# Performance work log

Hardware: AMD Instinct MI355X
Metric: run time of the kernel (lower is better)

The kernel has to match this reference:

```python
import jax, jax.numpy as jnp
import numpy as np

N_NODES = 50000
N_EDGES = 800000
IN_C = 64
HID = 64
OUT_C = 64
N_GRAPHS = 64


def setup_inputs() -> dict:
    key = jax.random.key(0)
    ks = jax.random.split(key, 12)
    x = jax.random.normal(ks[0], (N_NODES, IN_C), dtype=jnp.float32)
    edge_index = jax.random.randint(ks[1], (2, N_EDGES), 0, N_NODES, dtype=jnp.int64)
    # sorted graph-id vector guaranteed to cover all N_GRAPHS segments
    batch = (jnp.arange(N_NODES, dtype=jnp.int64) * N_GRAPHS) // N_NODES
    s = 0.1
    W1_root = jax.random.normal(ks[2], (IN_C, HID), dtype=jnp.float32) * s
    W1_rel = jax.random.normal(ks[3], (IN_C, HID), dtype=jnp.float32) * s
    b1 = jnp.zeros((HID,), dtype=jnp.float32)
    W2_root = jax.random.normal(ks[4], (HID, OUT_C), dtype=jnp.float32) * s
    W2_rel = jax.random.normal(ks[5], (HID, OUT_C), dtype=jnp.float32) * s
    b2 = jnp.zeros((OUT_C,), dtype=jnp.float32)
    fc1_w = jax.random.normal(ks[6], (OUT_C, 8), dtype=jnp.float32) * s
    fc1_b = jnp.zeros((8,), dtype=jnp.float32)
    fc2_w = jax.random.normal(ks[7], (8, 2), dtype=jnp.float32) * s
    fc2_b = jnp.zeros((2,), dtype=jnp.float32)
    return {
        "x": x, "edge_index": edge_index, "batch": batch,
        "W1_root": W1_root, "W1_rel": W1_rel, "b1": b1,
        "W2_root": W2_root, "W2_rel": W2_rel, "b2": b2,
        "fc1_w": fc1_w, "fc1_b": fc1_b, "fc2_w": fc2_w, "fc2_b": fc2_b,
    }


def _graph_conv(h, src, dst, W_root, W_rel, b, n_nodes):
    # PyG GraphConv (aggr='add'): out_i = W_root h_i + W_rel * sum_{j->i} h_j + b
    agg = jax.ops.segment_sum(h[src], dst, num_segments=n_nodes)
    return h @ W_root + agg @ W_rel + b


def reference(x, edge_index, batch, W1_root, W1_rel, b1,
              W2_root, W2_rel, b2, fc1_w, fc1_b, fc2_w, fc2_b):
    n = x.shape[0]
    src, dst = edge_index[0], edge_index[1]
    h = jax.nn.relu(_graph_conv(x, src, dst, W1_root, W1_rel, b1, n))
    h = jax.nn.relu(_graph_conv(h, src, dst, W2_root, W2_rel, b2, n))
    # mid = softmax over first 8 feature columns (split(8,1)[0])
    mid = jax.nn.softmax(h[:, :8], axis=1)
    z = jax.nn.relu(h @ fc1_w + fc1_b)
    z = jax.nn.relu(z @ fc2_w + fc2_b)
    pooled = jax.ops.segment_max(z, batch, num_segments=N_GRAPHS)  # global_max_pool
    out = jax.nn.softmax(pooled, axis=1)
    return (mid, out)
```

## Files before the change

### kernel.cpp

```cpp
#include <hip/hip_runtime.h>
#include <hip/hip_fp16.h>

typedef _Float16 f16_t;
typedef _Float16 f16x8 __attribute__((ext_vector_type(8)));
typedef float f32x4 __attribute__((ext_vector_type(4)));

#define N_NODES 50000
#define N_EDGES 800000
#define C 64
#define N_GRAPHS 64

#define NBKT 256
#define NPB 196
#define BKT_CAP 4096
#define HS_BLOCKS 256
#define HS_EPB (N_EDGES / HS_BLOCKS)
#define CAST_BLKS 1563
#define CUR_STRIDE 16

#define OFF_CUR    0u
#define OFF_POOLED 16384u
#define OFF_DONE   16896u
#define OFF_ROWS   17152u
#define OFF_ESRC   417280u
#define OFF_EPK    4611584u
#define OFF_XH     8805888u
#define OFF_H1H    15205888u
#define OFF_AGGH   21605888u
#define OFF_WT1    28005888u
#define OFF_WT2    28022272u

__device__ __forceinline__ unsigned pack2h(float x, float y) {
    __half2 h = __floats2half2_rn(x, y);
    return *reinterpret_cast<unsigned*>(&h);
}

__global__ __launch_bounds__(256) void init_cast_wcast_kernel(
        const float* __restrict__ x, f16_t* __restrict__ xh,
        const float* __restrict__ W1r, const float* __restrict__ W1l, f16_t* __restrict__ Wt1,
        const float* __restrict__ W2r, const float* __restrict__ W2l, f16_t* __restrict__ Wt2,
        int* __restrict__ cur, unsigned int* __restrict__ pooled,
        unsigned int* __restrict__ done_cnt) {
    __shared__ float w0[64 * 64];
    __shared__ float w1[64 * 64];
    const int blk = blockIdx.x;
    const int t = threadIdx.x;
    if (blk < CAST_BLKS) {
        if (blk == 0) {
            #pragma unroll
            for (int k = 0; k < CUR_STRIDE; k++) cur[k * 256 + t] = 0;
            if (t < N_GRAPHS * 2) pooled[t] = 0u;
            if (t == 0) *done_cnt = 0u;
        }
        const int i = blk * 256 + t;
        if (i < N_NODES * C / 8) {
            const float4* p = (const float4*)(x + (size_t)i * 8);
            float4 a = p[0], b = p[1];
            uint4 w;
            w.x = pack2h(a.x, a.y);
            w.y = pack2h(a.z, a.w);
            w.z = pack2h(b.x, b.y);
            w.w = pack2h(b.z, b.w);
            *(uint4*)(xh + (size_t)i * 8) = w;
        }
    } else {
        const int which = blk - CAST_BLKS;
        const float* Wr = which ? W2r : W1r;
        const float* Wl = which ? W2l : W1l;
        f16_t* Wt = which ? Wt2 : Wt1;
        for (int i = t * 4; i < 4096; i += 1024) {
            *(float4*)&w0[i] = *(const float4*)&Wr[i];
            *(float4*)&w1[i] = *(const float4*)&Wl[i];
        }
        __syncthreads();
        const int n = t >> 2, q = t & 3;
        for (int kk = q * 32; kk < q * 32 + 32; kk++) {
            float v = (kk < 64) ? w0[kk * 64 + n] : w1[(kk - 64) * 64 + n];
            Wt[n * 128 + kk] = (f16_t)v;
        }
    }
}

__global__ __launch_bounds__(256) void hist_scatter_kernel(const int* __restrict__ src,
                                                           const int* __restrict__ dst,
                                                           int* __restrict__ cur,
                                                           int* __restrict__ epk) {
    __shared__ int h[NBKT];
    __shared__ int base_s[NBKT];
    const int t = threadIdx.x;
    const int blk = blockIdx.x;
    h[t] = 0;
    __syncthreads();
    const int beg = blk * HS_EPB;
    for (int i = beg + t; i < beg + HS_EPB; i += 256)
        atomicAdd(&h[dst[i] / NPB], 1);
    __syncthreads();
    {
        int hv = h[t];
        int old = hv ? atomicAdd(&cur[t * CUR_STRIDE], hv) : 0;
        base_s[t] = t * BKT_CAP + old;
        h[t] = 0;
    }
    __syncthreads();
    for (int i = beg + t; i < beg + HS_EPB; i += 256) {
        int d = dst[i];
        int b = d / NPB;
        int off = atomicAdd(&h[b], 1);
        int pos = base_s[b] + off;
        if (pos < (b + 1) * BKT_CAP)
            epk[pos] = src[i] | ((d - b * NPB) << 16);
    }
}

__global__ __launch_bounds__(256) void fine_sort_kernel(const int* __restrict__ epk,
                                                        const int* __restrict__ cur,
                                                        int* __restrict__ esrc,
                                                        int2* __restrict__ rows) {
    __shared__ int cnt_s[NPB];
    __shared__ int s[256];
    __shared__ int staged[BKT_CAP];
    const int t = threadIdx.x;
    const int blk = blockIdx.x;
    const int base = blk * BKT_CAP;
    int n = cur[blk * CUR_STRIDE];
    if (n > BKT_CAP) n = BKT_CAP;
    if (t < NPB) cnt_s[t] = 0;
    __syncthreads();
    for (int e = t; e < n; e += 256)
        atomicAdd(&cnt_s[((unsigned)epk[base + e]) >> 16], 1);
    __syncthreads();
    int v = (t < NPB) ? cnt_s[t] : 0;
    s[t] = v;
    __syncthreads();
    for (int off = 1; off < 256; off <<= 1) {
        int x = (t >= off) ? s[t - off] : 0;
        __syncthreads();
        if (t >= off) s[t] += x;
        __syncthreads();
    }
    int excl = s[t] - v;
    const int node = blk * NPB + t;
    if (t < NPB) {
        cnt_s[t] = excl;
        if (node < N_NODES) {
            int2 be; be.x = base + excl; be.y = base + excl + v;
            rows[node] = be;
        }
    }
    __syncthreads();
    for (int e = t; e < n; e += 256) {
        int pk = epk[base + e];
        int pos = atomicAdd(&cnt_s[((unsigned)pk) >> 16], 1);
        staged[pos] = pk & 0xFFFF;
    }
    __syncthreads();
    for (int i = t; i < n; i += 256) esrc[base + i] = staged[i];
}

__global__ __launch_bounds__(256) void agg_kernel(const f16_t* __restrict__ hh,
                                                  const int2* __restrict__ rows,
                                                  const int* __restrict__ esrc,
                                                  f16_t* __restrict__ aggh) {
    const int wid = (blockIdx.x * 256 + threadIdx.x) >> 6;
    const int lane = threadIdx.x & 63;
    if (wid >= N_NODES) return;
    const int slot = lane >> 4;
    const int j = lane & 15;
    const uint2* hw = (const uint2*)hh;
    int2 be = rows[wid];
    int beg = be.x, end = be.y;
    float s0 = 0.f, s1 = 0.f, s2 = 0.f, s3 = 0.f;
    int e = beg;
    for (; e + 16 <= end; e += 16) {
        int i0 = esrc[e + slot];
        int i1 = esrc[e + 4 + slot];
        int i2 = esrc[e + 8 + slot];
        int i3 = esrc[e + 12 + slot];
        uint2 u0 = hw[(size_t)i0 * 16 + j];
        uint2 u1 = hw[(size_t)i1 * 16 + j];
        uint2 u2 = hw[(size_t)i2 * 16 + j];
        uint2 u3 = hw[(size_t)i3 * 16 + j];
        float2 a, b;
        a = __half22float2(*(__half2*)&u0.x); b = __half22float2(*(__half2*)&u0.y);
        s0 += a.x; s1 += a.y; s2 += b.x; s3 += b.y;
        a = __half22float2(*(__half2*)&u1.x); b = __half22float2(*(__half2*)&u1.y);
        s0 += a.x; s1 += a.y; s2 += b.x; s3 += b.y;
        a = __half22float2(*(__half2*)&u2.x); b = __half22float2(*(__half2*)&u2.y);
        s0 += a.x; s1 += a.y; s2 += b.x; s3 += b.y;
        a = __half22float2(*(__half2*)&u3.x); b = __half22float2(*(__half2*)&u3.y);
        s0 += a.x; s1 += a.y; s2 += b.x; s3 += b.y;
    }
    for (; e + 4 <= end; e += 4) {
        int i = esrc[e + slot];
        uint2 u = hw[(size_t)i * 16 + j];
        float2 a = __half22float2(*(__half2*)&u.x);
        float2 b = __half22float2(*(__half2*)&u.y);
        s0 += a.x; s1 += a.y; s2 += b.x; s3 += b.y;
    }
    int rem = end - e;
    if (slot < rem) {
        int i = esrc[e + slot];
        uint2 u = hw[(size_t)i * 16 + j];
        float2 a = __half22float2(*(__half2*)&u.x);
        float2 b = __half22float2(*(__half2*)&u.y);
        s0 += a.x; s1 += a.y; s2 += b.x; s3 += b.y;
    }
    s0 += __shfl_xor(s0, 16); s1 += __shfl_xor(s1, 16);
    s2 += __shfl_xor(s2, 16); s3 += __shfl_xor(s3, 16);
    s0 += __shfl_xor(s0, 32); s1 += __shfl_xor(s1, 32);
    s2 += __shfl_xor(s2, 32); s3 += __shfl_xor(s3, 32);
    if (slot == 0) {
        uint2 o;
        o.x = pack2h(s0, s1);
        o.y = pack2h(s2, s3);
        ((uint2*)aggh)[(size_t)wid * 16 + j] = o;
    }
}

__global__ __launch_bounds__(256) void gemm_mfma_kernel(const f16_t* __restrict__ Ah,
                                                        const f16_t* __restrict__ Bh,
                                                        const f16_t* __restrict__ Wt,
                                                        const float* __restrict__ bias,
                                                        f16_t* __restrict__ out16) {
    __shared__ f16_t Als[64 * 128];
    __shared__ f16_t Wls[64 * 128];
    const int t = threadIdx.x;
    const int row0 = blockIdx.x * 64;
    const int r = t >> 2, q = t & 3;
    int gr = row0 + r; if (gr > N_NODES - 1) gr = N_NODES - 1;
    const f16_t* srcA = (q < 2) ? &Ah[(size_t)gr * 64 + q * 32]
                                : &Bh[(size_t)gr * 64 + (q - 2) * 32];
    const f16_t* srcW = &Wt[r * 128 + q * 32];
    #pragma unroll
    for (int cc = 0; cc < 4; cc++) {
        const int c = q * 4 + cc;
        uint4 va = *(const uint4*)(srcA + cc * 8);
        uint4 vw = *(const uint4*)(srcW + cc * 8);
        *(uint4*)((char*)Als + r * 256 + ((c * 16) ^ ((r & 7) << 4))) = va;
        *(uint4*)((char*)Wls + r * 256 + ((c * 16) ^ ((r & 7) << 4))) = vw;
    }
    __syncthreads();
    const int w = t >> 6, l = t & 63;
    const int lr = l & 15, kh = l >> 4;
    const int arow = w * 16 + lr;
    f32x4 acc[4];
    #pragma unroll
    for (int nt = 0; nt < 4; nt++) {
        float b = bias[nt * 16 + lr];
        acc[nt] = (f32x4){b, b, b, b};
    }
    #pragma unroll
    for (int kt = 0; kt < 4; kt++) {
        const int kb = (kt * 32 + kh * 8) * 2;
        f16x8 a = *(const f16x8*)((const char*)Als + arow * 256 + (kb ^ ((arow & 7) << 4)));
        #pragma unroll
        for (int nt = 0; nt < 4; nt++) {
            const int n = nt * 16 + lr;
            f16x8 b = *(const f16x8*)((const char*)Wls + n * 256 + (kb ^ ((n & 7) << 4)));
            acc[nt] = __builtin_amdgcn_mfma_f32_16x16x32_f16(a, b, acc[nt], 0, 0, 0);
        }
    }
    #pragma unroll
    for (int nt = 0; nt < 4; nt++) {
        const int col = nt * 16 + lr;
        #pragma unroll
        for (int rr = 0; rr < 4; rr++) {
            const int gm = row0 + w * 16 + kh * 4 + rr;
            if (gm < N_NODES)
                out16[(size_t)gm * 64 + col] = (f16_t)fmaxf(acc[nt][rr], 0.f);
        }
    }
}

__global__ __launch_bounds__(256) void gemm2_head_kernel(
        const f16_t* __restrict__ Ah, const f16_t* __restrict__ Bh,
        const f16_t* __restrict__ Wt, const float* __restrict__ bias,
        const int* __restrict__ batch,
        const float* __restrict__ fc1w, const float* __restrict__ fc1b,
        const float* __restrict__ fc2w, const float* __restrict__ fc2b,
        float* __restrict__ mid_out, unsigned int* __restrict__ pooled,
        unsigned int* __restrict__ done_cnt, float* __restrict__ fin_out) {
    __shared__ f16_t Als[64 * 128];
    __shared__ f16_t Wls[64 * 128];
    __shared__ float tile[64 * 65];
    __shared__ float w1s[512];
    __shared__ float z1s[64 * 9];
    __shared__ float b1s[8];
    __shared__ float w2s[16];
    __shared__ float b2s[2];
    __shared__ unsigned int pool_s[N_GRAPHS * 2];
    __shared__ unsigned int amLast;
    __shared__ float fin[N_GRAPHS * 2];
    const int t = threadIdx.x;
    const int row0 = blockIdx.x * 64;
    const int r = t >> 2, q = t & 3;
    int gr = row0 + r; if (gr > N_NODES - 1) gr = N_NODES - 1;
    const f16_t* srcA = (q < 2) ? &Ah[(size_t)gr * 64 + q * 32]
                                : &Bh[(size_t)gr * 64 + (q - 2) * 32];
    const f16_t* srcW = &Wt[r * 128 + q * 32];
    #pragma unroll
    for (int cc = 0; cc < 4; cc++) {
        const int c = q * 4 + cc;
        uint4 va = *(const uint4*)(srcA + cc * 8);
        uint4 vw = *(const uint4*)(srcW + cc * 8);
        *(uint4*)((char*)Als + r * 256 + ((c * 16) ^ ((r & 7) << 4))) = va;
        *(uint4*)((char*)Wls + r * 256 + ((c * 16) ^ ((r & 7) << 4))) = vw;
    }
    for (int i = t; i < 512; i += 256) w1s[i] = fc1w[i];
    if (t < 8) b1s[t] = fc1b[t];
    if (t < 16) w2s[t] = fc2w[t];
    if (t < 2) b2s[t] = fc2b[t];
    if (t < N_GRAPHS * 2) pool_s[t] = 0u;
    __syncthreads();
    const int w = t >> 6, l = t & 63;
    const int lr = l & 15, kh = l >> 4;
    const int arow = w * 16 + lr;
    f32x4 acc[4];
    #pragma unroll
    for (int nt = 0; nt < 4; nt++) {
        float b = bias[nt * 16 + lr];
        acc[nt] = (f32x4){b, b, b, b};
    }
    #pragma unroll
    for (int kt = 0; kt < 4; kt++) {
        const int kb = (kt * 32 + kh * 8) * 2;
        f16x8 a = *(const f16x8*)((const char*)Als + arow * 256 + (kb ^ ((arow & 7) << 4)));
        #pragma unroll
        for (int nt = 0; nt < 4; nt++) {
            const int n = nt * 16 + lr;
            f16x8 b = *(const f16x8*)((const char*)Wls + n * 256 + (kb ^ ((n & 7) << 4)));
            acc[nt] = __builtin_amdgcn_mfma_f32_16x16x32_f16(a, b, acc[nt], 0, 0, 0);
        }
    }
    #pragma unroll
    for (int nt = 0; nt < 4; nt++) {
        const int col = nt * 16 + lr;
        #pragma unroll
        for (int rr = 0; rr < 4; rr++)
            tile[(w * 16 + kh * 4 + rr) * 65 + col] = fmaxf(acc[nt][rr], 0.f);
    }
    __syncthreads();
    const int row = t & 63, qq = t >> 6;
    const int gm = row0 + row;
    const bool valid = gm < N_NODES;
    {
        float z0 = b1s[2 * qq], z1v = b1s[2 * qq + 1];
        for (int k = 0; k < 64; k++) {
            float a = tile[row * 65 + k];
            z0  += a * w1s[k * 8 + 2 * qq];
            z1v += a * w1s[k * 8 + 2 * qq + 1];
        }
        z1s[row * 9 + 2 * qq]     = fmaxf(z0, 0.f);
        z1s[row * 9 + 2 * qq + 1] = fmaxf(z1v, 0.f);
    }
    if (qq == 0 && valid) {
        float rv[8];
        #pragma unroll
        for (int c = 0; c < 8; c++) rv[c] = tile[row * 65 + c];
        float m = rv[0];
        #pragma unroll
        for (int c = 1; c < 8; c++) m = fmaxf(m, rv[c]);
        float ex[8], s = 0.f;
        #pragma unroll
        for (int c = 0; c < 8; c++) { ex[c] = __expf(rv[c] - m); s += ex[c]; }
        float inv = 1.f / s;
        float4 v0 = {ex[0] * inv, ex[1] * inv, ex[2] * inv, ex[3] * inv};
        float4 v1 = {ex[4] * inv, ex[5] * inv, ex[6] * inv, ex[7] * inv};
        *(float4*)&mid_out[(size_t)gm * 8]     = v0;
        *(float4*)&mid_out[(size_t)gm * 8 + 4] = v1;
    }
    __syncthreads();
    if (qq == 0 && valid) {
        float z20 = b2s[0], z21 = b2s[1];
        #pragma unroll
        for (int o = 0; o < 8; o++) {
            float z = z1s[row * 9 + o];
            z20 += z * w2s[o * 2];
            z21 += z * w2s[o * 2 + 1];
        }
        z20 = fmaxf(z20, 0.f);
        z21 = fmaxf(z21, 0.f);
        int b = batch[gm];
        atomicMax(&pool_s[b * 2 + 0], __float_as_uint(z20));
        atomicMax(&pool_s[b * 2 + 1], __float_as_uint(z21));
    }
    __syncthreads();
    if (t < N_GRAPHS * 2) {
        unsigned int v = pool_s[t];
        if (v) atomicMax(&pooled[t], v);
    }
    __syncthreads();
    if (t == 0) {
        __threadfence();
        unsigned int prev = atomicAdd(done_cnt, 1u);
        amLast = (prev == gridDim.x - 1) ? 1u : 0u;
    }
    __syncthreads();
    if (amLast) {
        if (t < N_GRAPHS * 2) fin[t] = __uint_as_float(atomicMax(&pooled[t], 0u));
        __syncthreads();
        if (t < N_GRAPHS) {
            float v0 = fin[2 * t], v1 = fin[2 * t + 1];
            float m = fmaxf(v0, v1);
            float e0 = __expf(v0 - m), e1 = __expf(v1 - m);
            float s = e0 + e1;
            fin_out[2 * t]     = e0 / s;
            fin_out[2 * t + 1] = e1 / s;
        }
    }
}

extern "C" void kernel_launch(void* const* d_in, const int* in_sizes, int n_in,
                              void* d_out, int out_size, void* d_ws, size_t ws_size,
                              hipStream_t stream) {
    const float* x    = (const float*)d_in[0];
    const int*   ei   = (const int*)d_in[1];
    const int*   batch= (const int*)d_in[2];
    const float* W1r  = (const float*)d_in[3];
    const float* W1l  = (const float*)d_in[4];
    const float* b1   = (const float*)d_in[5];
    const float* W2r  = (const float*)d_in[6];
    const float* W2l  = (const float*)d_in[7];
    const float* b2   = (const float*)d_in[8];
    const float* fc1w = (const float*)d_in[9];
    const float* fc1b = (const float*)d_in[10];
    const float* fc2w = (const float*)d_in[11];
    const float* fc2b = (const float*)d_in[12];

    const int* src = ei;
    const int* dst = ei + N_EDGES;

    char* ws = (char*)d_ws;
    int*    cur    = (int*)(ws + OFF_CUR);
    unsigned int* pooled   = (unsigned int*)(ws + OFF_POOLED);
    unsigned int* done_cnt = (unsigned int*)(ws + OFF_DONE);
    int2*   rows   = (int2*)(ws + OFF_ROWS);
    int*    esrc   = (int*)(ws + OFF_ESRC);
    int*    epk    = (int*)(ws + OFF_EPK);
    f16_t*  xh     = (f16_t*)(ws + OFF_XH);
    f16_t*  h1h    = (f16_t*)(ws + OFF_H1H);
    f16_t*  aggh   = (f16_t*)(ws + OFF_AGGH);
    f16_t*  Wt1    = (f16_t*)(ws + OFF_WT1);
    f16_t*  Wt2    = (f16_t*)(ws + OFF_WT2);

    float* mid_out = (float*)d_out;
    float* fin_out = (float*)d_out + (size_t)N_NODES * 8;

    init_cast_wcast_kernel<<<CAST_BLKS + 2, 256, 0, stream>>>(
        x, xh, W1r, W1l, Wt1, W2r, W2l, Wt2, cur, pooled, done_cnt);
    hist_scatter_kernel<<<HS_BLOCKS, 256, 0, stream>>>(src, dst, cur, epk);
    fine_sort_kernel<<<NBKT, 256, 0, stream>>>(epk, cur, esrc, rows);

    const int AB = (N_NODES + 3) / 4;
    const int GB = (N_NODES + 63) / 64;

    agg_kernel<<<AB, 256, 0, stream>>>(xh, rows, esrc, aggh);
    gemm_mfma_kernel<<<GB, 256, 0, stream>>>(xh, aggh, Wt1, b1, h1h);
    agg_kernel<<<AB, 256, 0, stream>>>(h1h, rows, esrc, aggh);
    gemm2_head_kernel<<<GB, 256, 0, stream>>>(h1h, aggh, Wt2, b2, batch,
                                              fc1w, fc1b, fc2w, fc2b,
                                              mid_out, pooled, done_cnt, fin_out);
}
```

Measured before the change: 114.4 us.

## Fuse neighbor aggregation into GEMM kernels using 1024-thread blocks

Drops the separate agg kernels. Each 1024-thread block of 16 waves now gathers and sums neighbor features for its 64 rows straight into shared memory, then each wave computes one 16x16 MFMA output tile. This removes two launches and the global round trip of the aggregated fp16 buffer. In exchange, large blocks can lower occupancy and scheduling flexibility for the irregular gather, and the tail after the gather waits on a block-wide barrier.

```diff
diff --git a/kernel.cpp b/kernel.cpp
--- a/kernel.cpp
+++ b/kernel.cpp
@@ -26,9 +26,8 @@
 #define OFF_EPK    4611584u
 #define OFF_XH     8805888u
 #define OFF_H1H    15205888u
-#define OFF_AGGH   21605888u
-#define OFF_WT1    28005888u
-#define OFF_WT2    28022272u
+#define OFF_WT1    21605888u
+#define OFF_WT2    21622272u
 
 __device__ __forceinline__ unsigned pack2h(float x, float y) {
     __half2 h = __floats2half2_rn(x, y);
@@ -157,123 +156,117 @@
     for (int i = t; i < n; i += 256) esrc[base + i] = staged[i];
 }
 
-__global__ __launch_bounds__(256) void agg_kernel(const f16_t* __restrict__ hh,
-                                                  const int2* __restrict__ rows,
-                                                  const int* __restrict__ esrc,
-                                                  f16_t* __restrict__ aggh) {
-    const int wid = (blockIdx.x * 256 + threadIdx.x) >> 6;
-    const int lane = threadIdx.x & 63;
-    if (wid >= N_NODES) return;
-    const int slot = lane >> 4;
-    const int j = lane & 15;
-    const uint2* hw = (const uint2*)hh;
-    int2 be = rows[wid];
-    int beg = be.x, end = be.y;
-    float s0 = 0.f, s1 = 0.f, s2 = 0.f, s3 = 0.f;
-    int e = beg;
-    for (; e + 16 <= end; e += 16) {
-        int i0 = esrc[e + slot];
-        int i1 = esrc[e + 4 + slot];
-        int i2 = esrc[e + 8 + slot];
-        int i3 = esrc[e + 12 + slot];
-        uint2 u0 = hw[(size_t)i0 * 16 + j];
-        uint2 u1 = hw[(size_t)i1 * 16 + j];
-        uint2 u2 = hw[(size_t)i2 * 16 + j];
-        uint2 u3 = hw[(size_t)i3 * 16 + j];
-        float2 a, b;
-        a = __half22float2(*(__half2*)&u0.x); b = __half22float2(*(__half2*)&u0.y);
-        s0 += a.x; s1 += a.y; s2 += b.x; s3 += b.y;
-        a = __half22float2(*(__half2*)&u1.x); b = __half22float2(*(__half2*)&u1.y);
-        s0 += a.x; s1 += a.y; s2 += b.x; s3 += b.y;
-        a = __half22float2(*(__half2*)&u2.x); b = __half22float2(*(__half2*)&u2.y);
-        s0 += a.x; s1 += a.y; s2 += b.x; s3 += b.y;
-        a = __half22float2(*(__half2*)&u3.x); b = __half22float2(*(__half2*)&u3.y);
-        s0 += a.x; s1 += a.y; s2 += b.x; s3 += b.y;
-    }
-    for (; e + 4 <= end; e += 4) {
-        int i = esrc[e + slot];
-        uint2 u = hw[(size_t)i * 16 + j];
-        float2 a = __half22float2(*(__half2*)&u.x);
-        float2 b = __half22float2(*(__half2*)&u.y);
-        s0 += a.x; s1 += a.y; s2 += b.x; s3 += b.y;
-    }
-    int rem = end - e;
-    if (slot < rem) {
-        int i = esrc[e + slot];
-        uint2 u = hw[(size_t)i * 16 + j];
-        float2 a = __half22float2(*(__half2*)&u.x);
-        float2 b = __half22float2(*(__half2*)&u.y);
-        s0 += a.x; s1 += a.y; s2 += b.x; s3 += b.y;
-    }
-    s0 += __shfl_xor(s0, 16); s1 += __shfl_xor(s1, 16);
-    s2 += __shfl_xor(s2, 16); s3 += __shfl_xor(s3, 16);
-    s0 += __shfl_xor(s0, 32); s1 += __shfl_xor(s1, 32);
-    s2 += __shfl_xor(s2, 32); s3 += __shfl_xor(s3, 32);
-    if (slot == 0) {
-        uint2 o;
-        o.x = pack2h(s0, s1);
-        o.y = pack2h(s2, s3);
-        ((uint2*)aggh)[(size_t)wid * 16 + j] = o;
-    }
-}
-
-__global__ __launch_bounds__(256) void gemm_mfma_kernel(const f16_t* __restrict__ Ah,
-                                                        const f16_t* __restrict__ Bh,
-                                                        const f16_t* __restrict__ Wt,
-                                                        const float* __restrict__ bias,
-                                                        f16_t* __restrict__ out16) {
+__device__ __forceinline__ void stage_and_mfma(
+        const f16_t* __restrict__ Hsrc,
+        const int2* __restrict__ rows, const int* __restrict__ esrc,
+        const f16_t* __restrict__ Wt, const float* __restrict__ bias,
+        f16_t* Als, f16_t* Wls, int row0, int t, f32x4& acc,
+        int& ncol, int& outrow0) {
+    const int xr = t >> 4, xc = t & 15;
+    int gxr = row0 + xr; if (gxr > N_NODES - 1) gxr = N_NODES - 1;
+    uint2 xv = *(const uint2*)(Hsrc + (size_t)gxr * 64 + xc * 4);
+    uint4 wvv = *(const uint4*)(Wt + (t >> 4) * 128 + (t & 15) * 8);
+    const int wv = t >> 6, lane = t & 63;
+    const int slot = lane >> 4, j = lane & 15;
+    const uint2* hw = (const uint2*)Hsrc;
+    #pragma unroll
+    for (int i = 0; i < 4; i++) {
+        const int n = row0 + wv * 4 + i;
+        float s0 = 0.f, s1 = 0.f, s2 = 0.f, s3 = 0.f;
+        if (n < N_NODES) {
+            int2 be = rows[n];
+            int beg = be.x, end = be.y;
+            int e = beg;
+            for (; e + 16 <= end; e += 16) {
+                int i0 = esrc[e + slot];
+                int i1 = esrc[e + 4 + slot];
+                int i2 = esrc[e + 8 + slot];
+                int i3 = esrc[e + 12 + slot];
+                uint2 u0 = hw[(size_t)i0 * 16 + j];
+                uint2 u1 = hw[(size_t)i1 * 16 + j];
+                uint2 u2 = hw[(size_t)i2 * 16 + j];
+                uint2 u3 = hw[(size_t)i3 * 16 + j];
+                float2 a, b;
+                a = __half22float2(*(__half2*)&u0.x); b = __half22float2(*(__half2*)&u0.y);
+                s0 += a.x; s1 += a.y; s2 += b.x; s3 += b.y;
+                a = __half22float2(*(__half2*)&u1.x); b = __half22float2(*(__half2*)&u1.y);
+                s0 += a.x; s1 += a.y; s2 += b.x; s3 += b.y;
+                a = __half22float2(*(__half2*)&u2.x); b = __half22float2(*(__half2*)&u2.y);
+                s0 += a.x; s1 += a.y; s2 += b.x; s3 += b.y;
+                a = __half22float2(*(__half2*)&u3.x); b = __half22float2(*(__half2*)&u3.y);
+                s0 += a.x; s1 += a.y; s2 += b.x; s3 += b.y;
+            }
+            for (; e + 4 <= end; e += 4) {
+                int i0 = esrc[e + slot];
+                uint2 u = hw[(size_t)i0 * 16 + j];
+                float2 a = __half22float2(*(__half2*)&u.x);
+                float2 b = __half22float2(*(__half2*)&u.y);
+                s0 += a.x; s1 += a.y; s2 += b.x; s3 += b.y;
+            }
+            int rem = end - e;
+            if (slot < rem) {
+                int i0 = esrc[e + slot];
+                uint2 u = hw[(size_t)i0 * 16 + j];
+                float2 a = __half22float2(*(__half2*)&u.x);
+                float2 b = __half22float2(*(__half2*)&u.y);
+                s0 += a.x; s1 += a.y; s2 += b.x; s3 += b.y;
+            }
+        }
+        s0 += __shfl_xor(s0, 16); s1 += __shfl_xor(s1, 16);
+        s2 += __shfl_xor(s2, 16); s3 += __shfl_xor(s3, 16);
+        s0 += __shfl_xor(s0, 32); s1 += __shfl_xor(s1, 32);
+        s2 += __shfl_xor(s2, 32); s3 += __shfl_xor(s3, 32);
+        if (slot == 0) {
+            const int r = wv * 4 + i;
+            uint2 o; o.x = pack2h(s0, s1); o.y = pack2h(s2, s3);
+            *(uint2*)((char*)Als + r * 256 + ((128 + j * 8) ^ ((r & 7) << 4))) = o;
+        }
+    }
+    *(uint2*)((char*)Als + xr * 256 + ((xc * 8) ^ ((xr & 7) << 4))) = xv;
+    {
+        const int wn = t >> 4, wc8 = t & 15;
+        *(uint4*)((char*)Wls + wn * 256 + ((wc8 * 16) ^ ((wn & 7) << 4))) = wvv;
+    }
+    __syncthreads();
+    const int lr = lane & 15, kh = lane >> 4;
+    const int wr = wv >> 2, wc = wv & 3;
+    const int arow = wr * 16 + lr;
+    ncol = wc * 16 + lr;
+    outrow0 = row0 + wr * 16 + kh * 4;
+    float bv = bias[ncol];
+    acc = (f32x4){bv, bv, bv, bv};
+    #pragma unroll
+    for (int kt = 0; kt < 4; kt++) {
+        const int kb = (kt * 32 + kh * 8) * 2;
+        f16x8 a = *(const f16x8*)((const char*)Als + arow * 256 + (kb ^ ((arow & 7) << 4)));
+        f16x8 b = *(const f16x8*)((const char*)Wls + ncol * 256 + (kb ^ ((ncol & 7) << 4)));
+        acc = __builtin_amdgcn_mfma_f32_16x16x32_f16(a, b, acc, 0, 0, 0);
+    }
+}
+
+__global__ __launch_bounds__(1024) void layer1_kernel(const f16_t* __restrict__ xh,
+                                                      const int2* __restrict__ rows,
+                                                      const int* __restrict__ esrc,
+                                                      const f16_t* __restrict__ Wt,
+                                                      const float* __restrict__ bias,
+                                                      f16_t* __restrict__ h1h) {
     __shared__ f16_t Als[64 * 128];
     __shared__ f16_t Wls[64 * 128];
     const int t = threadIdx.x;
     const int row0 = blockIdx.x * 64;
-    const int r = t >> 2, q = t & 3;
-    int gr = row0 + r; if (gr > N_NODES - 1) gr = N_NODES - 1;
-    const f16_t* srcA = (q < 2) ? &Ah[(size_t)gr * 64 + q * 32]
-                                : &Bh[(size_t)gr * 64 + (q - 2) * 32];
-    const f16_t* srcW = &Wt[r * 128 + q * 32];
+    f32x4 acc; int ncol, outrow0;
+    stage_and_mfma(xh, rows, esrc, Wt, bias, Als, Wls, row0, t, acc, ncol, outrow0);
     #pragma unroll
-    for (int cc = 0; cc < 4; cc++) {
-        const int c = q * 4 + cc;
-        uint4 va = *(const uint4*)(srcA + cc * 8);
-        uint4 vw = *(const uint4*)(srcW + cc * 8);
-        *(uint4*)((char*)Als + r * 256 + ((c * 16) ^ ((r & 7) << 4))) = va;
-        *(uint4*)((char*)Wls + r * 256 + ((c * 16) ^ ((r & 7) << 4))) = vw;
-    }
-    __syncthreads();
-    const int w = t >> 6, l = t & 63;
-    const int lr = l & 15, kh = l >> 4;
-    const int arow = w * 16 + lr;
-    f32x4 acc[4];
-    #pragma unroll
-    for (int nt = 0; nt < 4; nt++) {
-        float b = bias[nt * 16 + lr];
-        acc[nt] = (f32x4){b, b, b, b};
-    }
-    #pragma unroll
-    for (int kt = 0; kt < 4; kt++) {
-        const int kb = (kt * 32 + kh * 8) * 2;
-        f16x8 a = *(const f16x8*)((const char*)Als + arow * 256 + (kb ^ ((arow & 7) << 4)));
-        #pragma unroll
-        for (int nt = 0; nt < 4; nt++) {
-            const int n = nt * 16 + lr;
-            f16x8 b = *(const f16x8*)((const char*)Wls + n * 256 + (kb ^ ((n & 7) << 4)));
-            acc[nt] = __builtin_amdgcn_mfma_f32_16x16x32_f16(a, b, acc[nt], 0, 0, 0);
-        }
-    }
-    #pragma unroll
-    for (int nt = 0; nt < 4; nt++) {
-        const int col = nt * 16 + lr;
-        #pragma unroll
-        for (int rr = 0; rr < 4; rr++) {
-            const int gm = row0 + w * 16 + kh * 4 + rr;
-            if (gm < N_NODES)
-                out16[(size_t)gm * 64 + col] = (f16_t)fmaxf(acc[nt][rr], 0.f);
-        }
-    }
-}
-
-__global__ __launch_bounds__(256) void gemm2_head_kernel(
-        const f16_t* __restrict__ Ah, const f16_t* __restrict__ Bh,
+    for (int rr = 0; rr < 4; rr++) {
+        const int gm = outrow0 + rr;
+        if (gm < N_NODES)
+            h1h[(size_t)gm * 64 + ncol] = (f16_t)fmaxf(acc[rr], 0.f);
+    }
+}
+
+__global__ __launch_bounds__(1024) void layer2_head_kernel(
+        const f16_t* __restrict__ h1h,
+        const int2* __restrict__ rows, const int* __restrict__ esrc,
         const f16_t* __restrict__ Wt, const float* __restrict__ bias,
         const int* __restrict__ batch,
         const float* __restrict__ fc1w, const float* __restrict__ fc1b,
@@ -293,57 +286,21 @@
     __shared__ float fin[N_GRAPHS * 2];
     const int t = threadIdx.x;
     const int row0 = blockIdx.x * 64;
-    const int r = t >> 2, q = t & 3;
-    int gr = row0 + r; if (gr > N_NODES - 1) gr = N_NODES - 1;
-    const f16_t* srcA = (q < 2) ? &Ah[(size_t)gr * 64 + q * 32]
-                                : &Bh[(size_t)gr * 64 + (q - 2) * 32];
-    const f16_t* srcW = &Wt[r * 128 + q * 32];
+    if (t < 512) w1s[t] = fc1w[t];
+    if (t >= 512 && t < 520) b1s[t - 512] = fc1b[t - 512];
+    if (t >= 520 && t < 536) w2s[t - 520] = fc2w[t - 520];
+    if (t >= 536 && t < 538) b2s[t - 536] = fc2b[t - 536];
+    if (t >= 544 && t < 544 + N_GRAPHS * 2) pool_s[t - 544] = 0u;
+    f32x4 acc; int ncol, outrow0;
+    stage_and_mfma(h1h, rows, esrc, Wt, bias, Als, Wls, row0, t, acc, ncol, outrow0);
     #pragma unroll
-    for (int cc = 0; cc < 4; cc++) {
-        const int c = q * 4 + cc;
-        uint4 va = *(const uint4*)(srcA + cc * 8);
-        uint4 vw = *(const uint4*)(srcW + cc * 8);
-        *(uint4*)((char*)Als + r * 256 + ((c * 16) ^ ((r & 7) << 4))) = va;
-        *(uint4*)((char*)Wls + r * 256 + ((c * 16) ^ ((r & 7) << 4))) = vw;
-    }
-    for (int i = t; i < 512; i += 256) w1s[i] = fc1w[i];
-    if (t < 8) b1s[t] = fc1b[t];
-    if (t < 16) w2s[t] = fc2w[t];
-    if (t < 2) b2s[t] = fc2b[t];
-    if (t < N_GRAPHS * 2) pool_s[t] = 0u;
-    __syncthreads();
-    const int w = t >> 6, l = t & 63;
-    const int lr = l & 15, kh = l >> 4;
-    const int arow = w * 16 + lr;
-    f32x4 acc[4];
-    #pragma unroll
-    for (int nt = 0; nt < 4; nt++) {
-        float b = bias[nt * 16 + lr];
-        acc[nt] = (f32x4){b, b, b, b};
-    }
-    #pragma unroll
-    for (int kt = 0; kt < 4; kt++) {
-        const int kb = (kt * 32 + kh * 8) * 2;
-        f16x8 a = *(const f16x8*)((const char*)Als + arow * 256 + (kb ^ ((arow & 7) << 4)));
-        #pragma unroll
-        for (int nt = 0; nt < 4; nt++) {
-            const int n = nt * 16 + lr;
-            f16x8 b = *(const f16x8*)((const char*)Wls + n * 256 + (kb ^ ((n & 7) << 4)));
-            acc[nt] = __builtin_amdgcn_mfma_f32_16x16x32_f16(a, b, acc[nt], 0, 0, 0);
-        }
-    }
-    #pragma unroll
-    for (int nt = 0; nt < 4; nt++) {
-        const int col = nt * 16 + lr;
-        #pragma unroll
-        for (int rr = 0; rr < 4; rr++)
-            tile[(w * 16 + kh * 4 + rr) * 65 + col] = fmaxf(acc[nt][rr], 0.f);
-    }
+    for (int rr = 0; rr < 4; rr++)
+        tile[(outrow0 - row0 + rr) * 65 + ncol] = fmaxf(acc[rr], 0.f);
     __syncthreads();
     const int row = t & 63, qq = t >> 6;
     const int gm = row0 + row;
     const bool valid = gm < N_NODES;
-    {
+    if (qq < 4) {
         float z0 = b1s[2 * qq], z1v = b1s[2 * qq + 1];
         for (int k = 0; k < 64; k++) {
             float a = tile[row * 65 + k];
@@ -353,7 +310,7 @@
         z1s[row * 9 + 2 * qq]     = fmaxf(z0, 0.f);
         z1s[row * 9 + 2 * qq + 1] = fmaxf(z1v, 0.f);
     }
-    if (qq == 0 && valid) {
+    if (qq == 4 && valid) {
         float rv[8];
         #pragma unroll
         for (int c = 0; c < 8; c++) rv[c] = tile[row * 65 + c];
@@ -439,7 +396,6 @@
     int*    epk    = (int*)(ws + OFF_EPK);
     f16_t*  xh     = (f16_t*)(ws + OFF_XH);
     f16_t*  h1h    = (f16_t*)(ws + OFF_H1H);
-    f16_t*  aggh   = (f16_t*)(ws + OFF_AGGH);
     f16_t*  Wt1    = (f16_t*)(ws + OFF_WT1);
     f16_t*  Wt2    = (f16_t*)(ws + OFF_WT2);
 
@@ -451,13 +407,10 @@
     hist_scatter_kernel<<<HS_BLOCKS, 256, 0, stream>>>(src, dst, cur, epk);
     fine_sort_kernel<<<NBKT, 256, 0, stream>>>(epk, cur, esrc, rows);
 
-    const int AB = (N_NODES + 3) / 4;
     const int GB = (N_NODES + 63) / 64;
 
-    agg_kernel<<<AB, 256, 0, stream>>>(xh, rows, esrc, aggh);
-    gemm_mfma_kernel<<<GB, 256, 0, stream>>>(xh, aggh, Wt1, b1, h1h);
-    agg_kernel<<<AB, 256, 0, stream>>>(h1h, rows, esrc, aggh);
-    gemm2_head_kernel<<<GB, 256, 0, stream>>>(h1h, aggh, Wt2, b2, batch,
-                                              fc1w, fc1b, fc2w, fc2b,
-                                              mid_out, pooled, done_cnt, fin_out);
-}
+    layer1_kernel<<<GB, 1024, 0, stream>>>(xh, rows, esrc, Wt1, b1, h1h);
+    layer2_head_kernel<<<GB, 1024, 0, stream>>>(h1h, rows, esrc, Wt2, b2, batch,
+                                                fc1w, fc1b, fc2w, fc2b,
+                                                mid_out, pooled, done_cnt, fin_out);
+}
```

Result: faster. 108.6 us (-5.1%).
